# Optimization experiments

Hardware: AMD Instinct MI355X
Metric: run time of the kernel (lower is better)

Reference implementation:

```python
import jax, jax.numpy as jnp
import numpy as np

M, N, D = 131072, 4000, 16

def setup_inputs() -> dict:
    key = jax.random.key(0)
    k1, k2, k3 = jax.random.split(key, 3)
    cse_embedding = jax.random.normal(k1, (M, D), dtype=jnp.float32)
    verts_colors = jax.random.uniform(k2, (N, 3), dtype=jnp.float32)
    verts_cse_embedding = jax.random.normal(k3, (N, D), dtype=jnp.float32)
    return {
        "cse_embedding": cse_embedding,
        "verts_colors": verts_colors,
        "verts_cse_embedding": verts_cse_embedding,
    }

def reference(cse_embedding, verts_colors, verts_cse_embedding):
    # Nearest neighbor in Euclidean distance == argmin of squared distance.
    # scores: (M, N)
    y_sq = jnp.sum(verts_cse_embedding * verts_cse_embedding, axis=-1)  # (N,)
    scores = y_sq[None, :] - 2.0 * jnp.einsum('md,nd->mn', cse_embedding, verts_cse_embedding)
    closest_verts = jnp.argmin(scores, axis=-1)  # (M,) int
    rendered_colors = verts_colors[closest_verts]  # (M, 3) gather
    return rendered_colors
```

## Files before the change

### kernel.cpp

```cpp
#include <hip/hip_runtime.h>
#include <math.h>
#include <stdint.h>

#define M_ROWS   131072
#define N_VERTS  4000
#define N_PAD    4096
#define D_DIM    16
#define N_TILES  (N_PAD / 16)
#define CHUNK_T  16
#define CHUNK_B  (CHUNK_T * 1024)
#define N_CHUNKS (N_TILES / CHUNK_T)

#define SCORE_BIAS 128.0f
#define TIE_EPS 0.025f

#define WS_YFRAG_OFF 0
#define WS_YSQ_OFF   262144
#define WS_CNT_OFF   278528
#define WS_LIST_OFF  278592

typedef float f32x4 __attribute__((ext_vector_type(4)));
typedef short s16x8 __attribute__((ext_vector_type(8)));

__device__ __forceinline__ unsigned short f32_to_bf16_rne(float f) {
    unsigned int u = __float_as_uint(f);
    u = (u + 0x7fffu + ((u >> 16) & 1u)) >> 16;
    return (unsigned short)u;
}
__device__ __forceinline__ float bf16_to_f32(unsigned short h) {
    return __uint_as_float(((unsigned int)h) << 16);
}
__device__ __forceinline__ uint32_t umin32(uint32_t a, uint32_t b) { return a < b ? a : b; }
__device__ __forceinline__ uint32_t umax32(uint32_t a, uint32_t b) { return a > b ? a : b; }

__global__ void pack_y_kernel(const float* __restrict__ verts,
                              char* __restrict__ yfrag,
                              float* __restrict__ ysq,
                              int* __restrict__ cnt) {
    const int tid = blockIdx.x * blockDim.x + threadIdx.x;
    if (tid == 0) *cnt = 0;

    {
        const int T = tid >> 6;
        const int l = tid & 63;
        const int q = l >> 4;
        const int c = l & 15;
        const int n = T * 16 + c;
        float v[8];
        if (n < N_VERTS) {
            const float* y = verts + (size_t)n * D_DIM + (q & 1) * 8;
#pragma unroll
            for (int j = 0; j < 8; ++j) v[j] = y[j];
        } else {
#pragma unroll
            for (int j = 0; j < 8; ++j) v[j] = 0.f;
        }
        s16x8 f;
        const bool lo = (q >= 2);
#pragma unroll
        for (int j = 0; j < 8; ++j) {
            const unsigned short hh = f32_to_bf16_rne(v[j]);
            unsigned short r = hh;
            if (lo) r = f32_to_bf16_rne(v[j] - bf16_to_f32(hh));
            f[j] = (short)r;
        }
        *(s16x8*)(yfrag + (size_t)tid * 16) = f;
    }

    if (tid < N_PAD) {
        float ys;
        if (tid < N_VERTS) {
            ys = SCORE_BIAS;
            const float* y = verts + (size_t)tid * D_DIM;
#pragma unroll
            for (int d = 0; d < D_DIM; ++d) ys = fmaf(y[d], y[d], ys);
        } else {
            ys = 1e30f;
        }
        ysq[tid] = ys;
    }
}

__global__ __launch_bounds__(512, 6) void mfma_screen_kernel(
    const float* __restrict__ x_all,
    const float* __restrict__ colors,
    const char* __restrict__ yfrag,
    const float* __restrict__ ysqg,
    float* __restrict__ out,
    int* __restrict__ cnt,
    int* __restrict__ list,
    int list_cap)
{
    __shared__ __align__(16) char  s_buf[2 * CHUNK_B];
    __shared__ __align__(16) float s_ysq[N_PAD];

    const int tid  = threadIdx.x;
    const int wave = tid >> 6;
    const int lane = tid & 63;
    const int q = lane >> 4;
    const int c = lane & 15;
    const int rowBase = blockIdx.x * 128 + wave * 16;

    const float* xr = x_all + (size_t)(rowBase + c) * D_DIM + (q & 1) * 8;
    const float4 xa = *(const float4*)xr;
    const float4 xb = *(const float4*)(xr + 4);
    const float xv[8] = {xa.x, xa.y, xa.z, xa.w, xb.x, xb.y, xb.z, xb.w};
    s16x8 a1, a2;
#pragma unroll
    for (int j = 0; j < 8; ++j) {
        const float a = -2.0f * xv[j];
        const unsigned short hh = f32_to_bf16_rne(a);
        a1[j] = (short)hh;
        a2[j] = (short)f32_to_bf16_rne(a - bf16_to_f32(hh));
    }

    {
        const int4* g = (const int4*)ysqg;
        int4* s = (int4*)s_ysq;
        s[tid] = g[tid];
        s[tid + 512] = g[tid + 512];
    }
    const int4* gy = (const int4*)yfrag;
    int4 ra = gy[tid];
    int4 rb = gy[512 + tid];
    {
        int4* s = (int4*)s_buf;
        s[tid] = ra;
        s[512 + tid] = rb;
    }

    uint32_t best[4]   = {0xFFFFFFFFu, 0xFFFFFFFFu, 0xFFFFFFFFu, 0xFFFFFFFFu};
    uint32_t second[4] = {0xFFFFFFFFu, 0xFFFFFFFFu, 0xFFFFFFFFu, 0xFFFFFFFFu};

    for (int ch = 0; ch < N_CHUNKS; ++ch) {
        if (ch + 1 < N_CHUNKS) {
            ra = gy[(ch + 1) * 1024 + tid];
            rb = gy[(ch + 1) * 1024 + 512 + tid];
        }
        __syncthreads();

        const char*  bb    = s_buf + (ch & 1) * CHUNK_B + lane * 16;
        const float* ysrow = s_ysq + ch * CHUNK_T * 16 + c;
#pragma unroll
        for (int t = 0; t < CHUNK_T; ++t) {
            const s16x8 bf = *(const s16x8*)(bb + t * 1024);
            const float ys = ysrow[t * 16];
            f32x4 acc = {ys, ys, ys, ys};
            acc = __builtin_amdgcn_mfma_f32_16x16x32_bf16(a1, bf, acc, 0, 0, 0);
            acc = __builtin_amdgcn_mfma_f32_16x16x32_bf16(a2, bf, acc, 0, 0, 0);
            const uint32_t tcur = (uint32_t)(ch * CHUNK_T + t);
#pragma unroll
            for (int r = 0; r < 4; ++r) {
                const uint32_t kb = (__float_as_uint(acc[r]) & 0xFFFFFF00u) | tcur;
                const uint32_t ob = best[r];
                second[r] = umin32(second[r], umax32(ob, kb));
                best[r]   = umin32(ob, kb);
            }
        }
        if (ch + 1 < N_CHUNKS) {
            int4* s = (int4*)(s_buf + ((ch + 1) & 1) * CHUNK_B);
            s[tid] = ra;
            s[512 + tid] = rb;
        }
    }

    __syncthreads();
    uint32_t* s_red  = (uint32_t*)s_buf;
    uint32_t* s_red2 = (uint32_t*)(s_buf + 8192);
#pragma unroll
    for (int r = 0; r < 4; ++r) {
        const int row = q * 4 + r;
        s_red [wave * 256 + row * 16 + c] = best[r];
        s_red2[wave * 256 + row * 16 + c] = second[r];
    }
    __syncthreads();

    if (lane < 16) {
        const int row = lane;
        uint32_t b1 = 0xFFFFFFFFu, b2 = 0xFFFFFFFFu, smin = 0xFFFFFFFFu;
        int cwin = 0;
#pragma unroll
        for (int cc = 0; cc < 16; ++cc) {
            const uint32_t k  = s_red [wave * 256 + row * 16 + cc];
            const uint32_t s2 = s_red2[wave * 256 + row * 16 + cc];
            smin = umin32(smin, s2);
            cwin = (k < b1) ? cc : cwin;
            b2 = umin32(b2, umax32(b1, k));
            b1 = umin32(b1, k);
        }
        const uint32_t secondAll = umin32(smin, b2);
        const float s1 = __uint_as_float(b1 & 0xFFFFFF00u);
        const float s2 = __uint_as_float(secondAll & 0xFFFFFF00u);
        const int n = (int)(b1 & 0xFFu) * 16 + cwin;
        const int m = rowBase + row;

        bool amb = (s2 - s1 <= TIE_EPS);
        if (amb) {
            const int pos = atomicAdd(cnt, 1);
            if (pos < list_cap) list[pos] = m;
            else amb = false;
        }
        if (!amb) {
            const float* cc2 = colors + (size_t)n * 3;
            float* o = out + (size_t)m * 3;
            o[0] = cc2[0];
            o[1] = cc2[1];
            o[2] = cc2[2];
        }
    }
}

__global__ __launch_bounds__(256) void rescan_kernel(
    const float* __restrict__ x_all,
    const float* __restrict__ colors,
    const float* __restrict__ verts,
    const int* __restrict__ cnt,
    const int* __restrict__ list,
    int list_cap,
    float* __restrict__ out)
{
    const int wavesPerBlock = blockDim.x >> 6;
    const int wid  = blockIdx.x * wavesPerBlock + (threadIdx.x >> 6);
    const int lane = threadIdx.x & 63;
    const int nWaves = gridDim.x * wavesPerBlock;

    int ccount = *cnt;
    if (ccount > list_cap) ccount = list_cap;

    for (int rr = wid; rr < ccount; rr += nWaves) {
        const int m = list[rr];
        double bx[D_DIM];
#pragma unroll
        for (int d = 0; d < D_DIM; ++d)
            bx[d] = (double)x_all[(size_t)m * D_DIM + d];

        double best = INFINITY;
        int bi = 0x7fffffff;
#pragma unroll 2
        for (int n = lane; n < N_VERTS; n += 64) {
            const float* y = verts + (size_t)n * D_DIM;
            double dot = 0.0, ys = 0.0;
#pragma unroll
            for (int d = 0; d < D_DIM; ++d) {
                const double yd = (double)y[d];
                dot = fma(bx[d], yd, dot);
                ys  = fma(yd, yd, ys);
            }
            const double s = ys - 2.0 * dot;
            if (s < best || (s == best && n < bi)) { best = s; bi = n; }
        }
#pragma unroll
        for (int off = 32; off > 0; off >>= 1) {
            const double ob = __shfl_xor(best, off, 64);
            const int    oi = __shfl_xor(bi, off, 64);
            if (ob < best || (ob == best && oi < bi)) { best = ob; bi = oi; }
        }
        if (lane == 0) {
            const float* cc = colors + (size_t)bi * 3;
            float* o = out + (size_t)m * 3;
            o[0] = cc[0];
            o[1] = cc[1];
            o[2] = cc[2];
        }
    }
}

extern "C" void kernel_launch(void* const* d_in, const int* in_sizes, int n_in,
                              void* d_out, int out_size, void* d_ws, size_t ws_size,
                              hipStream_t stream) {
    const float* cse_embedding       = (const float*)d_in[0];
    const float* verts_colors        = (const float*)d_in[1];
    const float* verts_cse_embedding = (const float*)d_in[2];
    float* out = (float*)d_out;

    char* ws = (char*)d_ws;
    char*  yfrag = ws + WS_YFRAG_OFF;
    float* ysq   = (float*)(ws + WS_YSQ_OFF);
    int*   cnt   = (int*)(ws + WS_CNT_OFF);
    int*   list  = (int*)(ws + WS_LIST_OFF);
    int list_cap = (int)((ws_size > WS_LIST_OFF)
                         ? ((ws_size - WS_LIST_OFF) / sizeof(int)) : 0);
    if (list_cap > M_ROWS) list_cap = M_ROWS;

    pack_y_kernel<<<(N_TILES * 64) / 256, 256, 0, stream>>>(
        verts_cse_embedding, yfrag, ysq, cnt);

    mfma_screen_kernel<<<M_ROWS / 128, 512, 0, stream>>>(
        cse_embedding, verts_colors, yfrag, ysq, out, cnt, list, list_cap);

    rescan_kernel<<<2048, 256, 0, stream>>>(
        cse_embedding, verts_colors, verts_cse_embedding, cnt, list,
        list_cap, out);
}
```

Measured before the change: 202.1 us.

## Switch screening to 32x32x16 MFMA with ysq folded into an extra MFMA

Replaces the 16x16x32 bf16 MFMA tiles with 32x32x16 tiles, so each wave screens 32 rows against 32 vertices per step. The y-squared bias is packed as a bf16 hi/lo pair and added through a fourth MFMA against a ones vector, which removes the shared ysq table and the per-tile LDS scalar loads. The low-part term is restructured into an explicit three-product split (a1*yh + a2*yh + a1*yl). Each thread now keeps 16 best/second registers and the block covers 256 rows, which raises register pressure and lowers the occupancy target from 6 to 4 waves per SIMD. The tie epsilon is widened slightly to absorb the bf16 rounding of ysq, which may send more rows to the rescan pass.

```diff
diff --git a/kernel.cpp b/kernel.cpp
--- a/kernel.cpp
+++ b/kernel.cpp
@@ -6,21 +6,21 @@
 #define N_VERTS  4000
 #define N_PAD    4096
 #define D_DIM    16
-#define N_TILES  (N_PAD / 16)
-#define CHUNK_T  16
-#define CHUNK_B  (CHUNK_T * 1024)
+#define N_TILES  (N_PAD / 32)
+#define TILE_B   3072
+#define CHUNK_T  8
+#define CHUNK_B  (CHUNK_T * TILE_B)
 #define N_CHUNKS (N_TILES / CHUNK_T)
 
 #define SCORE_BIAS 128.0f
-#define TIE_EPS 0.025f
+#define TIE_EPS 0.03f
 
 #define WS_YFRAG_OFF 0
-#define WS_YSQ_OFF   262144
-#define WS_CNT_OFF   278528
-#define WS_LIST_OFF  278592
-
-typedef float f32x4 __attribute__((ext_vector_type(4)));
-typedef short s16x8 __attribute__((ext_vector_type(8)));
+#define WS_CNT_OFF   393216
+#define WS_LIST_OFF  393280
+
+typedef float f32x16 __attribute__((ext_vector_type(16)));
+typedef short s16x8  __attribute__((ext_vector_type(8)));
 
 __device__ __forceinline__ unsigned short f32_to_bf16_rne(float f) {
     unsigned int u = __float_as_uint(f);
@@ -35,73 +35,76 @@
 
 __global__ void pack_y_kernel(const float* __restrict__ verts,
                               char* __restrict__ yfrag,
-                              float* __restrict__ ysq,
                               int* __restrict__ cnt) {
     const int tid = blockIdx.x * blockDim.x + threadIdx.x;
     if (tid == 0) *cnt = 0;
 
-    {
-        const int T = tid >> 6;
-        const int l = tid & 63;
-        const int q = l >> 4;
-        const int c = l & 15;
-        const int n = T * 16 + c;
-        float v[8];
+    const int T   = tid >> 6;
+    const int l   = tid & 63;
+    const int col = l & 31;
+    const int h   = l >> 5;
+    const int n   = T * 32 + col;
+    const int d0  = h * 8;
+
+    float v[8];
+    if (n < N_VERTS) {
+        const float* y = verts + (size_t)n * D_DIM + d0;
+#pragma unroll
+        for (int j = 0; j < 8; ++j) v[j] = y[j];
+    } else {
+#pragma unroll
+        for (int j = 0; j < 8; ++j) v[j] = 0.f;
+    }
+    s16x8 fh, fl;
+#pragma unroll
+    for (int j = 0; j < 8; ++j) {
+        const unsigned short hh = f32_to_bf16_rne(v[j]);
+        fh[j] = (short)hh;
+        fl[j] = (short)f32_to_bf16_rne(v[j] - bf16_to_f32(hh));
+    }
+    char* tb = yfrag + (size_t)T * TILE_B + (size_t)l * 16;
+    *(s16x8*)(tb)        = fh;
+    *(s16x8*)(tb + 1024) = fl;
+
+    s16x8 fy;
+#pragma unroll
+    for (int j = 0; j < 8; ++j) fy[j] = 0;
+    if (h == 0) {
+        float ys;
         if (n < N_VERTS) {
-            const float* y = verts + (size_t)n * D_DIM + (q & 1) * 8;
-#pragma unroll
-            for (int j = 0; j < 8; ++j) v[j] = y[j];
-        } else {
-#pragma unroll
-            for (int j = 0; j < 8; ++j) v[j] = 0.f;
-        }
-        s16x8 f;
-        const bool lo = (q >= 2);
-#pragma unroll
-        for (int j = 0; j < 8; ++j) {
-            const unsigned short hh = f32_to_bf16_rne(v[j]);
-            unsigned short r = hh;
-            if (lo) r = f32_to_bf16_rne(v[j] - bf16_to_f32(hh));
-            f[j] = (short)r;
-        }
-        *(s16x8*)(yfrag + (size_t)tid * 16) = f;
-    }
-
-    if (tid < N_PAD) {
-        float ys;
-        if (tid < N_VERTS) {
             ys = SCORE_BIAS;
-            const float* y = verts + (size_t)tid * D_DIM;
+            const float* y = verts + (size_t)n * D_DIM;
 #pragma unroll
             for (int d = 0; d < D_DIM; ++d) ys = fmaf(y[d], y[d], ys);
         } else {
             ys = 1e30f;
         }
-        ysq[tid] = ys;
-    }
-}
-
-__global__ __launch_bounds__(512, 6) void mfma_screen_kernel(
+        const unsigned short ysh = f32_to_bf16_rne(ys);
+        fy[0] = (short)ysh;
+        fy[1] = (short)f32_to_bf16_rne(ys - bf16_to_f32(ysh));
+    }
+    *(s16x8*)(tb + 2048) = fy;
+}
+
+__global__ __launch_bounds__(512, 4) void mfma_screen_kernel(
     const float* __restrict__ x_all,
     const float* __restrict__ colors,
     const char* __restrict__ yfrag,
-    const float* __restrict__ ysqg,
     float* __restrict__ out,
     int* __restrict__ cnt,
     int* __restrict__ list,
     int list_cap)
 {
-    __shared__ __align__(16) char  s_buf[2 * CHUNK_B];
-    __shared__ __align__(16) float s_ysq[N_PAD];
+    __shared__ __align__(16) char s_buf[2 * CHUNK_B];
 
     const int tid  = threadIdx.x;
     const int wave = tid >> 6;
     const int lane = tid & 63;
-    const int q = lane >> 4;
-    const int c = lane & 15;
-    const int rowBase = blockIdx.x * 128 + wave * 16;
-
-    const float* xr = x_all + (size_t)(rowBase + c) * D_DIM + (q & 1) * 8;
+    const int col  = lane & 31;
+    const int h    = lane >> 5;
+    const int rowBase = blockIdx.x * 256 + wave * 32;
+
+    const float* xr = x_all + (size_t)(rowBase + col) * D_DIM + h * 8;
     const float4 xa = *(const float4*)xr;
     const float4 xb = *(const float4*)(xr + 4);
     const float xv[8] = {xa.x, xa.y, xa.z, xa.w, xb.x, xb.y, xb.z, xb.w};
@@ -113,44 +116,50 @@
         a1[j] = (short)hh;
         a2[j] = (short)f32_to_bf16_rne(a - bf16_to_f32(hh));
     }
-
-    {
-        const int4* g = (const int4*)ysqg;
-        int4* s = (int4*)s_ysq;
-        s[tid] = g[tid];
-        s[tid + 512] = g[tid + 512];
-    }
+    s16x8 aone;
+#pragma unroll
+    for (int j = 0; j < 8; ++j) aone[j] = 0;
+    if (h == 0) { aone[0] = (short)0x3F80; aone[1] = (short)0x3F80; }
+
+    f32x16 zero16;
+#pragma unroll
+    for (int r = 0; r < 16; ++r) zero16[r] = 0.f;
+
     const int4* gy = (const int4*)yfrag;
     int4 ra = gy[tid];
     int4 rb = gy[512 + tid];
+    int4 rc = gy[1024 + tid];
     {
         int4* s = (int4*)s_buf;
-        s[tid] = ra;
-        s[512 + tid] = rb;
-    }
-
-    uint32_t best[4]   = {0xFFFFFFFFu, 0xFFFFFFFFu, 0xFFFFFFFFu, 0xFFFFFFFFu};
-    uint32_t second[4] = {0xFFFFFFFFu, 0xFFFFFFFFu, 0xFFFFFFFFu, 0xFFFFFFFFu};
+        s[tid] = ra; s[512 + tid] = rb; s[1024 + tid] = rc;
+    }
+
+    uint32_t best[16], second[16];
+#pragma unroll
+    for (int r = 0; r < 16; ++r) { best[r] = 0xFFFFFFFFu; second[r] = 0xFFFFFFFFu; }
 
     for (int ch = 0; ch < N_CHUNKS; ++ch) {
         if (ch + 1 < N_CHUNKS) {
-            ra = gy[(ch + 1) * 1024 + tid];
-            rb = gy[(ch + 1) * 1024 + 512 + tid];
+            const int base = (ch + 1) * 1536;
+            ra = gy[base + tid];
+            rb = gy[base + 512 + tid];
+            rc = gy[base + 1024 + tid];
         }
         __syncthreads();
 
-        const char*  bb    = s_buf + (ch & 1) * CHUNK_B + lane * 16;
-        const float* ysrow = s_ysq + ch * CHUNK_T * 16 + c;
+        const char* bb = s_buf + (ch & 1) * CHUNK_B + lane * 16;
 #pragma unroll
         for (int t = 0; t < CHUNK_T; ++t) {
-            const s16x8 bf = *(const s16x8*)(bb + t * 1024);
-            const float ys = ysrow[t * 16];
-            f32x4 acc = {ys, ys, ys, ys};
-            acc = __builtin_amdgcn_mfma_f32_16x16x32_bf16(a1, bf, acc, 0, 0, 0);
-            acc = __builtin_amdgcn_mfma_f32_16x16x32_bf16(a2, bf, acc, 0, 0, 0);
+            const s16x8 byh = *(const s16x8*)(bb + t * TILE_B);
+            const s16x8 byl = *(const s16x8*)(bb + t * TILE_B + 1024);
+            const s16x8 bys = *(const s16x8*)(bb + t * TILE_B + 2048);
+            f32x16 acc = __builtin_amdgcn_mfma_f32_32x32x16_bf16(a1, byh, zero16, 0, 0, 0);
+            acc = __builtin_amdgcn_mfma_f32_32x32x16_bf16(a2, byh, acc, 0, 0, 0);
+            acc = __builtin_amdgcn_mfma_f32_32x32x16_bf16(a1, byl, acc, 0, 0, 0);
+            acc = __builtin_amdgcn_mfma_f32_32x32x16_bf16(aone, bys, acc, 0, 0, 0);
             const uint32_t tcur = (uint32_t)(ch * CHUNK_T + t);
 #pragma unroll
-            for (int r = 0; r < 4; ++r) {
+            for (int r = 0; r < 16; ++r) {
                 const uint32_t kb = (__float_as_uint(acc[r]) & 0xFFFFFF00u) | tcur;
                 const uint32_t ob = best[r];
                 second[r] = umin32(second[r], umax32(ob, kb));
@@ -159,40 +168,50 @@
         }
         if (ch + 1 < N_CHUNKS) {
             int4* s = (int4*)(s_buf + ((ch + 1) & 1) * CHUNK_B);
-            s[tid] = ra;
-            s[512 + tid] = rb;
+            s[tid] = ra; s[512 + tid] = rb; s[1024 + tid] = rc;
         }
     }
 
     __syncthreads();
-    uint32_t* s_red  = (uint32_t*)s_buf;
-    uint32_t* s_red2 = (uint32_t*)(s_buf + 8192);
-#pragma unroll
-    for (int r = 0; r < 4; ++r) {
-        const int row = q * 4 + r;
-        s_red [wave * 256 + row * 16 + c] = best[r];
-        s_red2[wave * 256 + row * 16 + c] = second[r];
+    uint32_t* s_red = (uint32_t*)s_buf;
+#pragma unroll
+    for (int r = 0; r < 16; ++r) {
+        const int row = (r & 3) + 8 * (r >> 2) + 4 * h;
+        s_red[wave * 1024 + row * 32 + col] = best[r];
     }
     __syncthreads();
 
-    if (lane < 16) {
-        const int row = lane;
-        uint32_t b1 = 0xFFFFFFFFu, b2 = 0xFFFFFFFFu, smin = 0xFFFFFFFFu;
-        int cwin = 0;
-#pragma unroll
-        for (int cc = 0; cc < 16; ++cc) {
-            const uint32_t k  = s_red [wave * 256 + row * 16 + cc];
-            const uint32_t s2 = s_red2[wave * 256 + row * 16 + cc];
-            smin = umin32(smin, s2);
-            cwin = (k < b1) ? cc : cwin;
+    uint32_t b1 = 0xFFFFFFFFu, b2 = 0xFFFFFFFFu;
+    int cwin = 0;
+    if (tid < 256) {
+        const int w = tid >> 5, row = tid & 31;
+#pragma unroll
+        for (int c = 0; c < 32; ++c) {
+            const uint32_t k = s_red[w * 1024 + row * 32 + c];
+            cwin = (k < b1) ? c : cwin;
             b2 = umin32(b2, umax32(b1, k));
             b1 = umin32(b1, k);
         }
+    }
+    __syncthreads();
+#pragma unroll
+    for (int r = 0; r < 16; ++r) {
+        const int row = (r & 3) + 8 * (r >> 2) + 4 * h;
+        s_red[wave * 1024 + row * 32 + col] = second[r];
+    }
+    __syncthreads();
+
+    if (tid < 256) {
+        const int w = tid >> 5, row = tid & 31;
+        uint32_t smin = 0xFFFFFFFFu;
+#pragma unroll
+        for (int c = 0; c < 32; ++c)
+            smin = umin32(smin, s_red[w * 1024 + row * 32 + c]);
         const uint32_t secondAll = umin32(smin, b2);
         const float s1 = __uint_as_float(b1 & 0xFFFFFF00u);
         const float s2 = __uint_as_float(secondAll & 0xFFFFFF00u);
-        const int n = (int)(b1 & 0xFFu) * 16 + cwin;
-        const int m = rowBase + row;
+        const int n = (int)(b1 & 0xFFu) * 32 + cwin;
+        const int m = blockIdx.x * 256 + tid;
 
         bool amb = (s2 - s1 <= TIE_EPS);
         if (amb) {
@@ -275,7 +294,6 @@
 
     char* ws = (char*)d_ws;
     char*  yfrag = ws + WS_YFRAG_OFF;
-    float* ysq   = (float*)(ws + WS_YSQ_OFF);
     int*   cnt   = (int*)(ws + WS_CNT_OFF);
     int*   list  = (int*)(ws + WS_LIST_OFF);
     int list_cap = (int)((ws_size > WS_LIST_OFF)
@@ -283,10 +301,10 @@
     if (list_cap > M_ROWS) list_cap = M_ROWS;
 
     pack_y_kernel<<<(N_TILES * 64) / 256, 256, 0, stream>>>(
-        verts_cse_embedding, yfrag, ysq, cnt);
-
-    mfma_screen_kernel<<<M_ROWS / 128, 512, 0, stream>>>(
-        cse_embedding, verts_colors, yfrag, ysq, out, cnt, list, list_cap);
+        verts_cse_embedding, yfrag, cnt);
+
+    mfma_screen_kernel<<<M_ROWS / 256, 512, 0, stream>>>(
+        cse_embedding, verts_colors, yfrag, out, cnt, list, list_cap);
 
     rescan_kernel<<<2048, 256, 0, stream>>>(
         cse_embedding, verts_colors, verts_cse_embedding, cnt, list,
```

Measured after the change: 565.6 us. +179.9%, slower.
